# Optimization experiments

Measured on AMD Instinct MI355X. Metric: run time of the kernel, lower is better.

## Reference

```python
import jax, jax.numpy as jnp
import numpy as np
from math import sqrt

DIM = 2048
N_HEADS = 2
HEAD_DIM = DIM // N_HEADS  # 1024 == RoPE dims (dim // 2)
ROPE_DIMS = DIM // 2
ROPE_BASE = 10000.0


def apply_rope(x, dims=ROPE_DIMS, base=ROPE_BASE, offset=0):
    # x: [B, H, L, Dh]; non-traditional (split-half) RoPE over sequence axis
    L = x.shape[-2]
    pos = jnp.arange(offset, offset + L, dtype=x.dtype)[:, None]          # [L,1]
    inv = jnp.exp(jnp.arange(0, dims, 2, dtype=x.dtype) * (-np.log(base) / dims))  # [dims//2]
    theta = pos * inv                                                      # [L, dims//2]
    cos, sin = jnp.cos(theta), jnp.sin(theta)
    h = dims // 2
    x1, x2 = x[..., :h], x[..., h:dims]
    rx1 = x1 * cos - x2 * sin
    rx2 = x1 * sin + x2 * cos
    if dims < x.shape[-1]:
        return jnp.concatenate([rx1, rx2, x[..., dims:]], axis=-1)
    return jnp.concatenate([rx1, rx2], axis=-1)


def setup_inputs() -> dict:
    key = jax.random.key(0)
    ks = jax.random.split(key, 6)
    B, L = 4, 2048
    x = jax.random.normal(ks[0], (B, L, DIM), dtype=jnp.float32)
    # causal additive mask
    causal = jnp.tril(jnp.ones((L, L), dtype=bool))
    mask = jnp.where(causal, 0.0, -1e9).astype(jnp.float32)
    s1 = 1.0 / sqrt(DIM)
    Wqkv_w = jax.random.normal(ks[1], (3 * DIM, DIM), dtype=jnp.float32) * s1
    Wqkv_b = jnp.zeros((3 * DIM,), dtype=jnp.float32)
    out_w = jax.random.normal(ks[2], (DIM, DIM), dtype=jnp.float32) * s1
    out_b = jnp.zeros((DIM,), dtype=jnp.float32)
    return {"x": x, "mask": mask, "Wqkv_w": Wqkv_w, "Wqkv_b": Wqkv_b,
            "out_w": out_w, "out_b": out_b}


def reference(x, mask, Wqkv_w, Wqkv_b, out_w, out_b):
    B, L, D = x.shape
    H, Dh = N_HEADS, HEAD_DIM
    qkv = x @ Wqkv_w.T + Wqkv_b                       # [B, L, 3D]
    q, k, v = jnp.split(qkv, 3, axis=-1)
    # b l (h d) -> b h l d
    split = lambda t: t.reshape(B, L, H, Dh).transpose(0, 2, 1, 3)
    q, k, v = split(q), split(k), split(v)
    q = apply_rope(q)
    k = apply_rope(k)
    scale = sqrt(1.0 / Dh)
    scores = jnp.einsum('bhld,bhkd->bhlk', q * scale, k)  # [B,H,L,L]
    scores = scores + mask                                 # additive causal mask
    probs = jax.nn.softmax(scores, axis=-1)
    vh = jnp.einsum('bhlk,bhkd->bhld', probs, v)
    vh = vh.transpose(0, 2, 1, 3).reshape(B, L, D)         # b h l d -> b l (h d)
    out = vh @ out_w.T + out_b
    return (out, k, v)
```

## Files before the change

kernel.cpp:

```cpp
#include <hip/hip_runtime.h>
#include <hip/hip_bf16.h>
#include <math.h>

typedef unsigned short u16;
typedef __attribute__((ext_vector_type(8))) __bf16 bf16x8;
typedef __attribute__((ext_vector_type(4))) float f32x4;

__device__ __forceinline__ u16 f2b(float f) {
  unsigned u = __builtin_bit_cast(unsigned, f);
  u += 0x7fffu + ((u >> 16) & 1u);
  return (u16)(u >> 16);
}
__device__ __forceinline__ float b2f(u16 h) {
  unsigned u = ((unsigned)h) << 16;
  return __builtin_bit_cast(float, u);
}

__device__ __forceinline__ void gld_lds16(const u16* g, u16* l) {
  __builtin_amdgcn_global_load_lds(
      (const __attribute__((address_space(1))) unsigned int*)g,
      (__attribute__((address_space(3))) unsigned int*)l, 16, 0, 0);
}

#define MFMA16(a, b, c) \
  c = __builtin_amdgcn_mfma_f32_16x16x32_bf16(a, b, c, 0, 0, 0)

template <class FC>
__device__ __forceinline__ void gemm128_body(const u16* A, int lda,
                                             const u16* B, int ldb, FC fc,
                                             int m0, int n0, int K) {
  __shared__ __align__(16) u16 As[128 * 64];
  __shared__ __align__(16) u16 Bs[128 * 64];
  const int tid = threadIdx.x;
  const int wave = tid >> 6;
  const int lane = tid & 63;
  const int srow = lane >> 3;
  const int scol = ((lane & 7) ^ srow) * 8;
  const int wm = (wave & 1) * 64;
  const int wn = (wave >> 1) * 64;
  const int fm = lane & 15;
  const int fs = fm & 7;

  const u16* Abase = A + (size_t)m0 * lda;
  const u16* Bbase = B + (size_t)n0 * ldb;
  const size_t aLane = (size_t)(wave * 8 + srow) * lda + scol;
  const size_t bLane = (size_t)(wave * 8 + srow) * ldb + scol;

  f32x4 acc[4][4];
#pragma unroll
  for (int i = 0; i < 4; ++i)
#pragma unroll
    for (int j = 0; j < 4; ++j) acc[i][j] = (f32x4){0.f, 0.f, 0.f, 0.f};

  for (int k0 = 0; k0 < K; k0 += 64) {
#pragma unroll
    for (int c = 0; c < 4; ++c) {
      gld_lds16(Abase + (aLane + (size_t)(c * 32) * lda + k0),
                &As[(c * 4 + wave) * 512]);
      gld_lds16(Bbase + (bLane + (size_t)(c * 32) * ldb + k0),
                &Bs[(c * 4 + wave) * 512]);
    }
    __syncthreads();
#pragma unroll
    for (int kk = 0; kk < 2; ++kk) {
      const int cb = kk * 4 + (lane >> 4);
      const int p8 = (cb ^ fs) * 8;
      bf16x8 af[4], bfr[4];
#pragma unroll
      for (int i = 0; i < 4; ++i)
        af[i] = *(const bf16x8*)&As[(wm + i * 16 + fm) * 64 + p8];
#pragma unroll
      for (int j = 0; j < 4; ++j)
        bfr[j] = *(const bf16x8*)&Bs[(wn + j * 16 + fm) * 64 + p8];
#pragma unroll
      for (int i = 0; i < 4; ++i)
#pragma unroll
        for (int j = 0; j < 4; ++j) MFMA16(af[i], bfr[j], acc[i][j]);
    }
    __syncthreads();
  }
  const int er = lane >> 4;
#pragma unroll
  for (int i = 0; i < 4; ++i)
#pragma unroll
    for (int j = 0; j < 4; ++j)
#pragma unroll
      for (int r = 0; r < 4; ++r) {
        int m = m0 + wm + i * 16 + er * 4 + r;
        int n = n0 + wn + j * 16 + fm;
        fc(m, n, acc[i][j][r]);
      }
}

template <class FC>
__device__ __forceinline__ void gemm256_body(const u16* A, int lda,
                                             const u16* B, int ldb, FC fc,
                                             int m0, int n0, int K) {
  __shared__ __align__(16) u16 As[2][16384];
  __shared__ __align__(16) u16 Bs[2][16384];
  const int tid = threadIdx.x;
  const int wave = tid >> 6;
  const int lane = tid & 63;
  const int wr = wave >> 2;
  const int wc = wave & 3;
  const int fm = lane & 15;
  const int cb4 = lane >> 4;
  const int fs = fm & 7;
  const int srow = lane >> 3;
  const int scol = ((lane & 7) ^ srow) * 8;

  const u16* Ab = A + (size_t)(m0 + srow) * lda + scol;
  const u16* Bb = B + (size_t)(n0 + srow) * ldb + scol;

  const int paRow = (wr * 128 + fm) * 64;
  const int pbRow = (wc * 64 + fm) * 64;
  const int q0 = (cb4 ^ fs) * 8;
  const int q1 = q0 ^ 32;

  f32x4 acc[8][4];
#pragma unroll
  for (int m = 0; m < 8; ++m)
#pragma unroll
    for (int n = 0; n < 4; ++n) acc[m][n] = (f32x4){0.f, 0.f, 0.f, 0.f};

  auto stA = [&](int bi, int h, int kg) {
    const u16* g = Ab + (size_t)(h * 128 + wave * 8) * lda + kg;
    gld_lds16(g, &As[bi][h * 8192 + wave * 512]);
    gld_lds16(g + (size_t)64 * lda, &As[bi][h * 8192 + (wave + 8) * 512]);
  };
  auto stB = [&](int bi, int h, int kg) {
    const u16* g = Bb + (size_t)(h * 128 + wave * 8) * ldb + kg;
    gld_lds16(g, &Bs[bi][h * 8192 + wave * 512]);
    gld_lds16(g + (size_t)64 * ldb, &Bs[bi][h * 8192 + (wave + 8) * 512]);
  };

  const int nkt = K >> 6;

  stB(0, 0, 0);
  stB(0, 1, 0);
  stA(0, 0, 0);
  stA(0, 1, 0);
  stB(1, 0, 64);
  stB(1, 1, 64);
  stA(1, 0, 64);
  asm volatile("s_waitcnt vmcnt(6)" ::: "memory");
  __builtin_amdgcn_s_barrier();

  int buf = 0;
  for (int T = 0; T < nkt; ++T, buf ^= 1) {
    const int kc = T * 64;
    const bool sA1 = (T + 1) < nkt;
    const bool sN2 = (T + 2) < nkt;
    bf16x8 af[8], bv[4][2];
#pragma unroll
    for (int m = 0; m < 8; ++m)
      af[m] = *(const bf16x8*)&As[buf][paRow + m * 1024 + q0];
#pragma unroll
    for (int n = 0; n < 4; ++n) {
      bv[n][0] = *(const bf16x8*)&Bs[buf][pbRow + n * 1024 + q0];
      bv[n][1] = *(const bf16x8*)&Bs[buf][pbRow + n * 1024 + q1];
    }
    if (sA1) stA(buf ^ 1, 1, kc + 64);
    __builtin_amdgcn_s_barrier();
    asm volatile("s_waitcnt lgkmcnt(0)" ::: "memory");
    __builtin_amdgcn_sched_barrier(0);
    __builtin_amdgcn_s_setprio(1);
#pragma unroll
    for (int m = 0; m < 8; ++m) {
      MFMA16(af[m], bv[0][0], acc[m][0]);
      MFMA16(af[m], bv[1][0], acc[m][1]);
    }
    __builtin_amdgcn_s_setprio(0);
    __builtin_amdgcn_s_barrier();
    if (sN2) stB(buf, 0, kc + 128);
    __builtin_amdgcn_s_barrier();
    __builtin_amdgcn_s_setprio(1);
#pragma unroll
    for (int m = 0; m < 8; ++m) {
      MFMA16(af[m], bv[2][0], acc[m][2]);
      MFMA16(af[m], bv[3][0], acc[m][3]);
    }
    __builtin_amdgcn_s_setprio(0);
    __builtin_amdgcn_s_barrier();
#pragma unroll
    for (int m = 0; m < 8; ++m)
      af[m] = *(const bf16x8*)&As[buf][paRow + m * 1024 + q1];
    if (sN2) stB(buf, 1, kc + 128);
    __builtin_amdgcn_s_barrier();
    asm volatile("s_waitcnt lgkmcnt(0)" ::: "memory");
    __builtin_amdgcn_sched_barrier(0);
    __builtin_amdgcn_s_setprio(1);
#pragma unroll
    for (int m = 0; m < 8; ++m) {
      MFMA16(af[m], bv[0][1], acc[m][0]);
      MFMA16(af[m], bv[1][1], acc[m][1]);
    }
    __builtin_amdgcn_s_setprio(0);
    __builtin_amdgcn_s_barrier();
    if (sN2) stA(buf, 0, kc + 128);
    __builtin_amdgcn_s_barrier();
    __builtin_amdgcn_s_setprio(1);
#pragma unroll
    for (int m = 0; m < 8; ++m) {
      MFMA16(af[m], bv[2][1], acc[m][2]);
      MFMA16(af[m], bv[3][1], acc[m][3]);
    }
    __builtin_amdgcn_s_setprio(0);
    if (sN2) {
      asm volatile("s_waitcnt vmcnt(6)" ::: "memory");
    } else if (sA1) {
      asm volatile("s_waitcnt vmcnt(0)" ::: "memory");
    }
    __builtin_amdgcn_s_barrier();
  }

  const int er = lane >> 4;
#pragma unroll
  for (int m = 0; m < 8; ++m)
#pragma unroll
    for (int n = 0; n < 4; ++n)
#pragma unroll
      for (int r = 0; r < 4; ++r)
        fc(m0 + wr * 128 + m * 16 + er * 4 + r, n0 + wc * 64 + n * 16 + fm,
           acc[m][n][r]);
}

struct EQKV {
  u16* qb;
  u16* kb;
  float* vout;
  const float* bias;
  __device__ __forceinline__ void operator()(int m, int n, float v) const {
    v += bias[n];
    int b = m >> 11, l = m & 2047;
    int part = n >> 11, nn = n & 2047, h = nn >> 10, d = nn & 1023;
    size_t idx = ((size_t)((b << 1) + h) * 2048 + l) * 1024 + d;
    if (part == 0)
      qb[idx] = f2b(v);
    else if (part == 1)
      kb[idx] = f2b(v);
    else
      vout[idx] = v;
  }
};
struct EScoreB {
  u16* S;
  __device__ __forceinline__ void operator()(int m, int n, float v) const {
    S[((size_t)m << 11) + n] = f2b(v * 0.03125f + (n > m ? -1.0e9f : 0.0f));
  }
};
struct EBf16 {
  u16* o;
  int ld;
  __device__ __forceinline__ void operator()(int m, int n, float v) const {
    o[(size_t)m * ld + n] = f2b(v);
  }
};
struct EOut {
  float* o;
  const float* bias;
  __device__ __forceinline__ void operator()(int m, int n, float v) const {
    o[((size_t)m << 11) + n] = v + bias[n];
  }
};

__device__ __forceinline__ u16* spz(u16* sp0, u16* sp1, int z) {
  return (z < 4) ? sp0 + (size_t)z * 4194304 : sp1 + (size_t)(z - 4) * 4194304;
}

__global__ void __launch_bounds__(256) k_cast3(const float* x, const float* w1,
                                               const float* w2, u16* xb,
                                               u16* w1b, u16* w2b) {
  long i = (long)(blockIdx.x * 256 + threadIdx.x) * 4;
  const float* src;
  u16* dst;
  long off;
  if (i < 16777216L) {
    src = x; dst = xb; off = i;
  } else if (i < 16777216L + 12582912L) {
    src = w1; dst = w1b; off = i - 16777216L;
  } else {
    src = w2; dst = w2b; off = i - 16777216L - 12582912L;
  }
  float4 f = *(const float4*)(src + off);
  ushort4 o;
  o.x = f2b(f.x);
  o.y = f2b(f.y);
  o.z = f2b(f.z);
  o.w = f2b(f.w);
  *(ushort4*)(dst + off) = o;
}

__global__ void __launch_bounds__(512, 2) k_qkv(const u16* xb, const u16* wb,
                                                const float* bias, u16* qb,
                                                u16* kb, float* vout) {
  gemm256_body(xb, 2048, wb, 2048, EQKV{qb, kb, vout, bias}, blockIdx.y * 256,
               blockIdx.x * 256, 2048);
}

__global__ void __launch_bounds__(256) k_rope(u16* qb, u16* kb, float* kout) {
  int l = blockIdx.x;
  int t = threadIdx.x;
  float lf = (float)l;
  const float c0 = (float)(-9.210340371976184 / 1024.0);
  float s0, c_0, s1, c_1;
  {
    float inv = __expf((float)(2 * t) * c0);
    __sincosf(lf * inv, &s0, &c_0);
    float inv2 = __expf((float)(2 * (t + 256)) * c0);
    __sincosf(lf * inv2, &s1, &c_1);
  }
#pragma unroll
  for (int bh = 0; bh < 8; ++bh) {
    size_t base = ((size_t)bh * 2048 + l) * 1024;
#pragma unroll
    for (int half = 0; half < 2; ++half) {
      int i = t + half * 256;
      float c = half ? c_1 : c_0;
      float s = half ? s1 : s0;
      float x1 = b2f(qb[base + i]), x2 = b2f(qb[base + 512 + i]);
      qb[base + i] = f2b(x1 * c - x2 * s);
      qb[base + 512 + i] = f2b(x1 * s + x2 * c);
      float y1 = b2f(kb[base + i]), y2 = b2f(kb[base + 512 + i]);
      float r1 = y1 * c - y2 * s, r2 = y1 * s + y2 * c;
      kb[base + i] = f2b(r1);
      kb[base + 512 + i] = f2b(r2);
      kout[base + i] = r1;
      kout[base + 512 + i] = r2;
    }
  }
}

__global__ void __launch_bounds__(256) k_transpose_v(const float* v, u16* vt) {
  __shared__ u16 tile[64][65];
  int bh = blockIdx.z;
  int d0 = blockIdx.x * 64, l0 = blockIdx.y * 64;
  const float* vb = v + (size_t)bh * 2048 * 1024;
  u16* vtb = vt + (size_t)bh * 1024 * 2048;
  int t = threadIdx.x;
  int c = t & 63, r4 = t >> 6;
#pragma unroll
  for (int r = 0; r < 16; ++r) {
    int row = r * 4 + r4;
    tile[row][c] = f2b(vb[(size_t)(l0 + row) * 1024 + d0 + c]);
  }
  __syncthreads();
#pragma unroll
  for (int r = 0; r < 16; ++r) {
    int drow = r * 4 + r4;
    vtb[(size_t)(d0 + drow) * 2048 + l0 + c] = tile[c][drow];
  }
}

__global__ void __launch_bounds__(256) k_score(const u16* qb, const u16* kb,
                                               u16* sp0, u16* sp1) {
  int m0 = blockIdx.y * 128, n0 = blockIdx.x * 128;
  if (n0 > m0) return;
  int z = blockIdx.z;
  const u16* q = qb + (size_t)z * 2048 * 1024;
  const u16* k = kb + (size_t)z * 2048 * 1024;
  gemm128_body(q, 1024, k, 1024, EScoreB{spz(sp0, sp1, z)}, m0, n0, 1024);
}

__global__ void __launch_bounds__(256) k_softmax(u16* sp0, u16* sp1) {
  int l = blockIdx.x, z = blockIdx.y;
  u16* row = spz(sp0, sp1, z) + ((size_t)l << 11);
  int t = threadIdx.x;
  int jend = ((l >> 8) + 1) << 8;
  __shared__ float red[4];
  float vals[8];
  float mx = -1e30f;
#pragma unroll
  for (int i = 0; i < 8; ++i) {
    int j = i * 256 + t;
    float v = (j <= l) ? b2f(row[j]) : -1e30f;
    vals[i] = v;
    mx = fmaxf(mx, v);
  }
#pragma unroll
  for (int off = 32; off; off >>= 1) mx = fmaxf(mx, __shfl_down(mx, off));
  if ((t & 63) == 0) red[t >> 6] = mx;
  __syncthreads();
  mx = fmaxf(fmaxf(red[0], red[1]), fmaxf(red[2], red[3]));
  __syncthreads();
  float sum = 0.f;
#pragma unroll
  for (int i = 0; i < 8; ++i) {
    int j = i * 256 + t;
    float e = (j <= l) ? __expf(vals[i] - mx) : 0.f;
    vals[i] = e;
    sum += e;
  }
#pragma unroll
  for (int off = 32; off; off >>= 1) sum += __shfl_down(sum, off);
  if ((t & 63) == 0) red[t >> 6] = sum;
  __syncthreads();
  sum = red[0] + red[1] + red[2] + red[3];
  float is = 1.0f / sum;
#pragma unroll
  for (int i = 0; i < 8; ++i) {
    int j = i * 256 + t;
    if (j < jend) row[j] = f2b(vals[i] * is);
  }
}

__global__ void __launch_bounds__(512, 2) k_pv(u16* sp0, u16* sp1,
                                               const u16* vt, u16* vh) {
  int z = blockIdx.z;
  int b = z >> 1, h = z & 1;
  int m0 = blockIdx.y * 256, n0 = blockIdx.x * 256;
  const u16* Pz = spz(sp0, sp1, z);
  const u16* vtb = vt + (size_t)z * 1024 * 2048;
  u16* outb = vh + (size_t)b * 2048 * 2048 + (size_t)h * 1024;
  int Keff = m0 + 256;
  gemm256_body(Pz, 2048, vtb, 2048, EBf16{outb, 2048}, m0, n0, Keff);
}

__global__ void __launch_bounds__(512, 2) k_out(const u16* vh, const u16* w2,
                                                const float* bias, float* out) {
  gemm256_body(vh, 2048, w2, 2048, EOut{out, bias}, blockIdx.y * 256,
               blockIdx.x * 256, 2048);
}

extern "C" void kernel_launch(void* const* d_in, const int* in_sizes, int n_in,
                              void* d_out, int out_size, void* d_ws,
                              size_t ws_size, hipStream_t stream) {
  const float* x = (const float*)d_in[0];
  const float* w1 = (const float*)d_in[2];
  const float* b1 = (const float*)d_in[3];
  const float* w2 = (const float*)d_in[4];
  const float* b2 = (const float*)d_in[5];
  float* out = (float*)d_out;
  float* kout = out + (size_t)16777216;
  float* vout = kout + (size_t)16777216;

  char* ws = (char*)d_ws;
  u16* xb = (u16*)ws;
  ws += (size_t)33554432;
  u16* w1b = (u16*)ws;
  ws += (size_t)25165824;
  u16* w2b = (u16*)ws;
  ws += (size_t)8388608;
  u16* qb = (u16*)ws;
  ws += (size_t)33554432;
  u16* kb = (u16*)ws;
  ws += (size_t)33554432;
  u16* vtb = (u16*)ws;
  ws += (size_t)33554432;
  u16* sp1 = (u16*)ws;
  u16* sp0 = xb;
  u16* vh = qb;

  k_cast3<<<32768, 256, 0, stream>>>(x, w1, w2, xb, w1b, w2b);
  k_qkv<<<dim3(24, 32), 512, 0, stream>>>(xb, w1b, b1, qb, kb, vout);
  k_rope<<<2048, 256, 0, stream>>>(qb, kb, kout);
  k_transpose_v<<<dim3(16, 32, 8), 256, 0, stream>>>(vout, vtb);
  k_score<<<dim3(16, 16, 8), 256, 0, stream>>>(qb, kb, sp0, sp1);
  k_softmax<<<dim3(2048, 8), 256, 0, stream>>>(sp0, sp1);
  k_pv<<<dim3(4, 8, 8), 512, 0, stream>>>(sp0, sp1, vtb, vh);
  k_out<<<dim3(8, 32), 512, 0, stream>>>(vh, w2b, b2, out);
}
```

Baseline: 807.8 us.

## Restructure 256-tile GEMM pipeline, vectorize RoPE, use 128 tiles for PV

The 256x256 GEMM main loop is reorganized so next-tile LDS fragment reads interleave with MFMAs via sched_group_barrier. Global-to-LDS loads are now issued in whole-tile groups, with fewer barriers per K step. RoPE now processes adjacent pairs with vectorized ushort2/float2 loads and stores. The PV GEMM switches to 128x128 tiles with 256 threads, giving finer causal granularity and more blocks. The cost is more register pressure from holding fragments across iterations, and more complex wait counts that could introduce hazards.

```diff
diff --git a/kernel.cpp b/kernel.cpp
--- a/kernel.cpp
+++ b/kernel.cpp
@@ -123,27 +123,41 @@
 #pragma unroll
     for (int n = 0; n < 4; ++n) acc[m][n] = (f32x4){0.f, 0.f, 0.f, 0.f};
 
-  auto stA = [&](int bi, int h, int kg) {
-    const u16* g = Ab + (size_t)(h * 128 + wave * 8) * lda + kg;
-    gld_lds16(g, &As[bi][h * 8192 + wave * 512]);
-    gld_lds16(g + (size_t)64 * lda, &As[bi][h * 8192 + (wave + 8) * 512]);
+  auto stA2 = [&](int bi, int kg) {
+#pragma unroll
+    for (int h = 0; h < 2; ++h) {
+      const u16* g = Ab + (size_t)(h * 128 + wave * 8) * lda + kg;
+      gld_lds16(g, &As[bi][h * 8192 + wave * 512]);
+      gld_lds16(g + (size_t)64 * lda, &As[bi][h * 8192 + (wave + 8) * 512]);
+    }
   };
-  auto stB = [&](int bi, int h, int kg) {
-    const u16* g = Bb + (size_t)(h * 128 + wave * 8) * ldb + kg;
-    gld_lds16(g, &Bs[bi][h * 8192 + wave * 512]);
-    gld_lds16(g + (size_t)64 * ldb, &Bs[bi][h * 8192 + (wave + 8) * 512]);
+  auto stB2 = [&](int bi, int kg) {
+#pragma unroll
+    for (int h = 0; h < 2; ++h) {
+      const u16* g = Bb + (size_t)(h * 128 + wave * 8) * ldb + kg;
+      gld_lds16(g, &Bs[bi][h * 8192 + wave * 512]);
+      gld_lds16(g + (size_t)64 * ldb, &Bs[bi][h * 8192 + (wave + 8) * 512]);
+    }
   };
 
   const int nkt = K >> 6;
 
-  stB(0, 0, 0);
-  stB(0, 1, 0);
-  stA(0, 0, 0);
-  stA(0, 1, 0);
-  stB(1, 0, 64);
-  stB(1, 1, 64);
-  stA(1, 0, 64);
-  asm volatile("s_waitcnt vmcnt(6)" ::: "memory");
+  stB2(0, 0);
+  stA2(0, 0);
+  stB2(1, 64);
+  stA2(1, 64);
+  asm volatile("s_waitcnt vmcnt(8)" ::: "memory");
+  __builtin_amdgcn_s_barrier();
+  bf16x8 af[8], bv[4][2];
+#pragma unroll
+  for (int m = 0; m < 8; ++m)
+    af[m] = *(const bf16x8*)&As[0][paRow + m * 1024 + q0];
+#pragma unroll
+  for (int n = 0; n < 4; ++n) {
+    bv[n][0] = *(const bf16x8*)&Bs[0][pbRow + n * 1024 + q0];
+    bv[n][1] = *(const bf16x8*)&Bs[0][pbRow + n * 1024 + q1];
+  }
+  asm volatile("s_waitcnt lgkmcnt(0)" ::: "memory");
   __builtin_amdgcn_s_barrier();
 
   int buf = 0;
@@ -151,66 +165,67 @@
     const int kc = T * 64;
     const bool sA1 = (T + 1) < nkt;
     const bool sN2 = (T + 2) < nkt;
-    bf16x8 af[8], bv[4][2];
-#pragma unroll
-    for (int m = 0; m < 8; ++m)
-      af[m] = *(const bf16x8*)&As[buf][paRow + m * 1024 + q0];
-#pragma unroll
-    for (int n = 0; n < 4; ++n) {
-      bv[n][0] = *(const bf16x8*)&Bs[buf][pbRow + n * 1024 + q0];
-      bv[n][1] = *(const bf16x8*)&Bs[buf][pbRow + n * 1024 + q1];
-    }
-    if (sA1) stA(buf ^ 1, 1, kc + 64);
-    __builtin_amdgcn_s_barrier();
-    asm volatile("s_waitcnt lgkmcnt(0)" ::: "memory");
+    if (sN2) stB2(buf, kc + 128);
     __builtin_amdgcn_sched_barrier(0);
     __builtin_amdgcn_s_setprio(1);
 #pragma unroll
     for (int m = 0; m < 8; ++m) {
       MFMA16(af[m], bv[0][0], acc[m][0]);
       MFMA16(af[m], bv[1][0], acc[m][1]);
+      MFMA16(af[m], bv[2][0], acc[m][2]);
+      MFMA16(af[m], bv[3][0], acc[m][3]);
+      af[m] = *(const bf16x8*)&As[buf][paRow + m * 1024 + q1];
+      __builtin_amdgcn_sched_group_barrier(0x008, 4, 0);
+      __builtin_amdgcn_sched_group_barrier(0x100, 1, 0);
     }
     __builtin_amdgcn_s_setprio(0);
+    asm volatile("s_waitcnt lgkmcnt(0)" ::: "memory");
     __builtin_amdgcn_s_barrier();
-    if (sN2) stB(buf, 0, kc + 128);
+    if (sN2) stA2(buf, kc + 128);
+    __builtin_amdgcn_sched_barrier(0);
+    if (sN2) {
+      asm volatile("s_waitcnt vmcnt(8)" ::: "memory");
+    } else if (sA1) {
+      asm volatile("s_waitcnt vmcnt(0)" ::: "memory");
+    }
     __builtin_amdgcn_s_barrier();
     __builtin_amdgcn_s_setprio(1);
-#pragma unroll
-    for (int m = 0; m < 8; ++m) {
-      MFMA16(af[m], bv[2][0], acc[m][2]);
-      MFMA16(af[m], bv[3][0], acc[m][3]);
+    if (sA1) {
+#pragma unroll
+      for (int m = 0; m < 4; ++m) {
+        MFMA16(af[m], bv[0][1], acc[m][0]);
+        MFMA16(af[m], bv[1][1], acc[m][1]);
+        MFMA16(af[m], bv[2][1], acc[m][2]);
+        MFMA16(af[m], bv[3][1], acc[m][3]);
+        af[m] = *(const bf16x8*)&As[buf ^ 1][paRow + m * 1024 + q0];
+        bv[m][0] = *(const bf16x8*)&Bs[buf ^ 1][pbRow + m * 1024 + q0];
+        __builtin_amdgcn_sched_group_barrier(0x008, 4, 0);
+        __builtin_amdgcn_sched_group_barrier(0x100, 2, 0);
+      }
+#pragma unroll
+      for (int m = 4; m < 8; ++m) {
+        MFMA16(af[m], bv[0][1], acc[m][0]);
+        MFMA16(af[m], bv[1][1], acc[m][1]);
+        MFMA16(af[m], bv[2][1], acc[m][2]);
+        MFMA16(af[m], bv[3][1], acc[m][3]);
+        af[m] = *(const bf16x8*)&As[buf ^ 1][paRow + m * 1024 + q0];
+        __builtin_amdgcn_sched_group_barrier(0x008, 4, 0);
+        __builtin_amdgcn_sched_group_barrier(0x100, 1, 0);
+      }
+#pragma unroll
+      for (int n = 0; n < 4; ++n)
+        bv[n][1] = *(const bf16x8*)&Bs[buf ^ 1][pbRow + n * 1024 + q1];
+    } else {
+#pragma unroll
+      for (int m = 0; m < 8; ++m) {
+        MFMA16(af[m], bv[0][1], acc[m][0]);
+        MFMA16(af[m], bv[1][1], acc[m][1]);
+        MFMA16(af[m], bv[2][1], acc[m][2]);
+        MFMA16(af[m], bv[3][1], acc[m][3]);
+      }
     }
     __builtin_amdgcn_s_setprio(0);
-    __builtin_amdgcn_s_barrier();
-#pragma unroll
-    for (int m = 0; m < 8; ++m)
-      af[m] = *(const bf16x8*)&As[buf][paRow + m * 1024 + q1];
-    if (sN2) stB(buf, 1, kc + 128);
-    __builtin_amdgcn_s_barrier();
     asm volatile("s_waitcnt lgkmcnt(0)" ::: "memory");
-    __builtin_amdgcn_sched_barrier(0);
-    __builtin_amdgcn_s_setprio(1);
-#pragma unroll
-    for (int m = 0; m < 8; ++m) {
-      MFMA16(af[m], bv[0][1], acc[m][0]);
-      MFMA16(af[m], bv[1][1], acc[m][1]);
-    }
-    __builtin_amdgcn_s_setprio(0);
-    __builtin_amdgcn_s_barrier();
-    if (sN2) stA(buf, 0, kc + 128);
-    __builtin_amdgcn_s_barrier();
-    __builtin_amdgcn_s_setprio(1);
-#pragma unroll
-    for (int m = 0; m < 8; ++m) {
-      MFMA16(af[m], bv[2][1], acc[m][2]);
-      MFMA16(af[m], bv[3][1], acc[m][3]);
-    }
-    __builtin_amdgcn_s_setprio(0);
-    if (sN2) {
-      asm volatile("s_waitcnt vmcnt(6)" ::: "memory");
-    } else if (sA1) {
-      asm volatile("s_waitcnt vmcnt(0)" ::: "memory");
-    }
     __builtin_amdgcn_s_barrier();
   }
 
@@ -303,31 +318,37 @@
   int t = threadIdx.x;
   float lf = (float)l;
   const float c0 = (float)(-9.210340371976184 / 1024.0);
-  float s0, c_0, s1, c_1;
+  float sa, ca, sb, cb;
   {
-    float inv = __expf((float)(2 * t) * c0);
-    __sincosf(lf * inv, &s0, &c_0);
-    float inv2 = __expf((float)(2 * (t + 256)) * c0);
-    __sincosf(lf * inv2, &s1, &c_1);
-  }
+    float inva = __expf((float)(4 * t) * c0);
+    __sincosf(lf * inva, &sa, &ca);
+    float invb = __expf((float)(4 * t + 2) * c0);
+    __sincosf(lf * invb, &sb, &cb);
+  }
+  const int d = 2 * t;
 #pragma unroll
   for (int bh = 0; bh < 8; ++bh) {
     size_t base = ((size_t)bh * 2048 + l) * 1024;
-#pragma unroll
-    for (int half = 0; half < 2; ++half) {
-      int i = t + half * 256;
-      float c = half ? c_1 : c_0;
-      float s = half ? s1 : s0;
-      float x1 = b2f(qb[base + i]), x2 = b2f(qb[base + 512 + i]);
-      qb[base + i] = f2b(x1 * c - x2 * s);
-      qb[base + 512 + i] = f2b(x1 * s + x2 * c);
-      float y1 = b2f(kb[base + i]), y2 = b2f(kb[base + 512 + i]);
-      float r1 = y1 * c - y2 * s, r2 = y1 * s + y2 * c;
-      kb[base + i] = f2b(r1);
-      kb[base + 512 + i] = f2b(r2);
-      kout[base + i] = r1;
-      kout[base + 512 + i] = r2;
-    }
+    ushort2 x1 = *(const ushort2*)&qb[base + d];
+    ushort2 x2 = *(const ushort2*)&qb[base + 512 + d];
+    float a1 = b2f(x1.x), a2 = b2f(x2.x);
+    float b1 = b2f(x1.y), b2 = b2f(x2.y);
+    ushort2 q1 = {f2b(a1 * ca - a2 * sa), f2b(b1 * cb - b2 * sb)};
+    ushort2 q2 = {f2b(a1 * sa + a2 * ca), f2b(b1 * sb + b2 * cb)};
+    *(ushort2*)&qb[base + d] = q1;
+    *(ushort2*)&qb[base + 512 + d] = q2;
+    ushort2 y1 = *(const ushort2*)&kb[base + d];
+    ushort2 y2 = *(const ushort2*)&kb[base + 512 + d];
+    float k1a = b2f(y1.x), k2a = b2f(y2.x);
+    float k1b = b2f(y1.y), k2b = b2f(y2.y);
+    float r1a = k1a * ca - k2a * sa, r2a = k1a * sa + k2a * ca;
+    float r1b = k1b * cb - k2b * sb, r2b = k1b * sb + k2b * cb;
+    ushort2 ka = {f2b(r1a), f2b(r1b)};
+    ushort2 kc = {f2b(r2a), f2b(r2b)};
+    *(ushort2*)&kb[base + d] = ka;
+    *(ushort2*)&kb[base + 512 + d] = kc;
+    *(float2*)&kout[base + d] = make_float2(r1a, r1b);
+    *(float2*)&kout[base + 512 + d] = make_float2(r2a, r2b);
   }
 }
 
@@ -404,16 +425,16 @@
   }
 }
 
-__global__ void __launch_bounds__(512, 2) k_pv(u16* sp0, u16* sp1,
-                                               const u16* vt, u16* vh) {
+__global__ void __launch_bounds__(256) k_pv(u16* sp0, u16* sp1, const u16* vt,
+                                            u16* vh) {
   int z = blockIdx.z;
   int b = z >> 1, h = z & 1;
-  int m0 = blockIdx.y * 256, n0 = blockIdx.x * 256;
+  int m0 = blockIdx.y * 128, n0 = blockIdx.x * 128;
   const u16* Pz = spz(sp0, sp1, z);
   const u16* vtb = vt + (size_t)z * 1024 * 2048;
   u16* outb = vh + (size_t)b * 2048 * 2048 + (size_t)h * 1024;
-  int Keff = m0 + 256;
-  gemm256_body(Pz, 2048, vtb, 2048, EBf16{outb, 2048}, m0, n0, Keff);
+  int Keff = m0 + 128;
+  gemm128_body(Pz, 2048, vtb, 2048, EBf16{outb, 2048}, m0, n0, Keff);
 }
 
 __global__ void __launch_bounds__(512, 2) k_out(const u16* vh, const u16* w2,
@@ -457,6 +478,6 @@
   k_transpose_v<<<dim3(16, 32, 8), 256, 0, stream>>>(vout, vtb);
   k_score<<<dim3(16, 16, 8), 256, 0, stream>>>(qb, kb, sp0, sp1);
   k_softmax<<<dim3(2048, 8), 256, 0, stream>>>(sp0, sp1);
-  k_pv<<<dim3(4, 8, 8), 512, 0, stream>>>(sp0, sp1, vtb, vh);
+  k_pv<<<dim3(8, 16, 8), 256, 0, stream>>>(sp0, sp1, vtb, vh);
   k_out<<<dim3(8, 32), 512, 0, stream>>>(vh, w2b, b2, out);
 }
```

Result: faster. 782.9 us (-3.1%).
